# Kernel optimization log

Hardware: AMD Instinct MI355X
Metric: run time of the kernel (lower is better)

The kernel has to match this reference:

```python
import jax, jax.numpy as jnp
import numpy as np

E, M, B, S = 1024, 256, 4, 2048
LN_EPS = 1e-5

def _l2norm(x):
    # F.normalize(p=2, dim=-1, eps=1e-12)
    n = jnp.linalg.norm(x, axis=-1, keepdims=True)
    return x / jnp.maximum(n, 1e-12)

def _layernorm(x, g, b):
    mu = jnp.mean(x, axis=-1, keepdims=True)
    var = jnp.var(x, axis=-1, keepdims=True)
    return (x - mu) * jax.lax.rsqrt(var + LN_EPS) * g + b

def setup_inputs() -> dict:
    key = jax.random.key(0)
    ks = jax.random.split(key, 16)
    s = 0.02
    inp = {
        'x': jax.random.normal(ks[0], (B, S, E), jnp.float32),
        'memory': jnp.zeros((B, M, M), jnp.float32),
        'w_k': jax.random.normal(ks[1], (M, E), jnp.float32) * s,
        'b_k': jnp.zeros((M,), jnp.float32),
        'w_q': jax.random.normal(ks[2], (M, E), jnp.float32) * s,
        'b_q': jnp.zeros((M,), jnp.float32),
        'w_v': jax.random.normal(ks[3], (M, E), jnp.float32) * s,
        'b_v': jnp.zeros((M,), jnp.float32),
        'w_out': jax.random.normal(ks[4], (E, M), jnp.float32) * s,
        'b_out': jnp.zeros((E,), jnp.float32),
        'w_gw': jax.random.normal(ks[5], (1, E), jnp.float32) * s,
        'b_gw': jnp.full((1,), -2.0, jnp.float32),
        'w_gf': jax.random.normal(ks[6], (1, E), jnp.float32) * s,
        'b_gf': jnp.full((1,), 2.0, jnp.float32),
        'ln1_g': jnp.ones((E,), jnp.float32),
        'ln1_b': jnp.zeros((E,), jnp.float32),
        'ln2_g': jnp.ones((E,), jnp.float32),
        'ln2_b': jnp.zeros((E,), jnp.float32),
        'w_f1': jax.random.normal(ks[7], (4 * E, E), jnp.float32) * s,
        'b_f1': jnp.zeros((4 * E,), jnp.float32),
        'w_f2': jax.random.normal(ks[8], (E, 4 * E), jnp.float32) * s,
        'b_f2': jnp.zeros((E,), jnp.float32),
    }
    return inp

def reference(x, memory, w_k, b_k, w_q, b_q, w_v, b_v, w_out, b_out,
              w_gw, b_gw, w_gf, b_gf, ln1_g, ln1_b, ln2_g, ln2_b,
              w_f1, b_f1, w_f2, b_f2):
    xn = _layernorm(x, ln1_g, ln1_b)                      # [B,S,E]
    k_all = _l2norm(xn @ w_k.T + b_k)                     # [B,S,M]
    q_all = _l2norm(xn @ w_q.T + b_q)                     # [B,S,M]
    v_all = jnp.tanh(xn @ w_v.T + b_v)                    # [B,S,M]
    beta_all = jax.nn.sigmoid(xn @ w_gw.T + b_gw)         # [B,S,1]
    decay_all = jax.nn.sigmoid(xn @ w_gf.T + b_gf)        # [B,S,1]

    def step(mem, inps):
        k, q, v, beta, decay = inps                       # k,q,v:[B,M]; beta,decay:[B,1]
        readout = jnp.einsum('bij,bj->bi', mem, q)        # read BEFORE update
        assoc = v[:, :, None] * k[:, None, :]             # [B,M,M] outer product
        mem = decay[:, :, None] * mem + beta[:, :, None] * assoc
        return mem, readout

    seq = (jnp.swapaxes(k_all, 0, 1), jnp.swapaxes(q_all, 0, 1),
           jnp.swapaxes(v_all, 0, 1), jnp.swapaxes(beta_all, 0, 1),
           jnp.swapaxes(decay_all, 0, 1))
    new_memory, readouts = jax.lax.scan(step, memory, seq)  # readouts: [S,B,M]
    stacked = jnp.swapaxes(readouts, 0, 1)                  # [B,S,M]
    mixer_out = stacked @ w_out.T + b_out                   # [B,S,E]

    x = x + mixer_out
    h = _layernorm(x, ln2_g, ln2_b)
    ffn = jax.nn.gelu(h @ w_f1.T + b_f1, approximate=False) @ w_f2.T + b_f2
    x = x + ffn
    return (x, new_memory)
```

## Files before the change

kernel.cpp:

```cpp
#include <hip/hip_runtime.h>
#include <stdint.h>

#define E_DIM 1024
#define M_DIM 256
#define B_DIM 4
#define S_DIM 2048
#define NTOK  8192
#define CHUNK 64
#define NCHUNK 32
#define NCB   128

typedef unsigned short u16;
typedef unsigned int   u32;
typedef __attribute__((ext_vector_type(8))) short short8;
typedef __attribute__((ext_vector_type(4))) float floatx4;

#define OFF_WKQV   ((size_t)0)
#define OFF_WOUT   ((size_t)1572864)
#define OFF_WF1    ((size_t)2097152)
#define OFF_WF2    ((size_t)10485760)
#define OFF_BKQV   ((size_t)18874368)
#define OFF_BETA   ((size_t)18877440)
#define OFF_DECAY  ((size_t)18910208)
#define OFF_P      ((size_t)18942976)
#define OFF_WW     ((size_t)18976256)
#define OFF_ABUF   ((size_t)19009024)
#define OFF_XN     ((size_t)21106176)
#define OFF_KQV    ((size_t)37883392)
#define OFF_T      ((size_t)63049216)
#define OFF_STATES ((size_t)96603648)
#define OFF_RO     ((size_t)130158080)
#define OFF_H      OFF_XN
#define OFF_Y1     OFF_T
#define OFF_G      OFF_STATES

__device__ __forceinline__ u16 f2bf(float f) {
    union { float f; u32 u; } a; a.f = f;
    u32 u = a.u;
    return (u16)((u + 0x7fffu + ((u >> 16) & 1u)) >> 16);
}
__device__ __forceinline__ u32 pack2bf(float a, float b) {
    return (u32)f2bf(a) | ((u32)f2bf(b) << 16);
}
__device__ __forceinline__ float sigmoidf_(float x) { return 1.0f / (1.0f + expf(-x)); }

__device__ __forceinline__ void gload_lds16(const u16* g, u16* l) {
    __builtin_amdgcn_global_load_lds((const __attribute__((address_space(1))) void*)g,
                                     (__attribute__((address_space(3))) void*)l, 16, 0, 0);
}

__device__ __forceinline__ void block_reduce_2(float& a, float& b, float* red, int t) {
#pragma unroll
    for (int o = 32; o > 0; o >>= 1) { a += __shfl_xor(a, o); b += __shfl_xor(b, o); }
    if ((t & 63) == 0) { red[t >> 6] = a; red[4 + (t >> 6)] = b; }
    __syncthreads();
    a = red[0] + red[1] + red[2] + red[3];
    b = red[4] + red[5] + red[6] + red[7];
    __syncthreads();
}

__global__ void f2bf4_kernel(const float4* __restrict__ in, uint2* __restrict__ out, int n4) {
    int i = blockIdx.x * 256 + threadIdx.x;
    if (i < n4) {
        float4 v = in[i];
        uint2 o; o.x = pack2bf(v.x, v.y); o.y = pack2bf(v.z, v.w);
        out[i] = o;
    }
}
__global__ void pack_kqv_w(const float4* __restrict__ wk, const float4* __restrict__ wq,
                           const float4* __restrict__ wv, uint2* __restrict__ out) {
    int i = blockIdx.x * 256 + threadIdx.x;
    int sec = i >> 16;
    int off = i & 65535;
    const float4* src = (sec == 0) ? wk : ((sec == 1) ? wq : wv);
    float4 v = src[off];
    uint2 o; o.x = pack2bf(v.x, v.y); o.y = pack2bf(v.z, v.w);
    out[i] = o;
}
__global__ void pack_bias(const float* __restrict__ bk, const float* __restrict__ bq,
                          const float* __restrict__ bv, float* __restrict__ out) {
    int i = blockIdx.x * 256 + threadIdx.x;
    if (i < 256) out[i] = bk[i];
    else if (i < 512) out[i] = bq[i - 256];
    else out[i] = bv[i - 512];
}

__global__ __launch_bounds__(256) void ln1_gates(
    const float* __restrict__ x, const float* __restrict__ g, const float* __restrict__ b,
    const float* __restrict__ wgw, const float* __restrict__ bgw,
    const float* __restrict__ wgf, const float* __restrict__ bgf,
    u16* __restrict__ xn, float* __restrict__ beta, float* __restrict__ decay)
{
    __shared__ float red[8];
    const int row = blockIdx.x;
    const int t = threadIdx.x;
    const float4 v = ((const float4*)(x + (size_t)row * E_DIM))[t];
    float s  = v.x + v.y + v.z + v.w;
    float ss = v.x * v.x + v.y * v.y + v.z * v.z + v.w * v.w;
    block_reduce_2(s, ss, red, t);
    const float mean = s * (1.0f / E_DIM);
    const float var  = ss * (1.0f / E_DIM) - mean * mean;
    const float rstd = rsqrtf(var + 1e-5f);
    const float4 gg = ((const float4*)g)[t];
    const float4 bb = ((const float4*)b)[t];
    float4 xnv;
    xnv.x = (v.x - mean) * rstd * gg.x + bb.x;
    xnv.y = (v.y - mean) * rstd * gg.y + bb.y;
    xnv.z = (v.z - mean) * rstd * gg.z + bb.z;
    xnv.w = (v.w - mean) * rstd * gg.w + bb.w;
    uint2 o; o.x = pack2bf(xnv.x, xnv.y); o.y = pack2bf(xnv.z, xnv.w);
    ((uint2*)(xn + (size_t)row * E_DIM))[t] = o;
    const float4 w1 = ((const float4*)wgw)[t];
    const float4 w2 = ((const float4*)wgf)[t];
    float dg = xnv.x * w1.x + xnv.y * w1.y + xnv.z * w1.z + xnv.w * w1.w;
    float df = xnv.x * w2.x + xnv.y * w2.y + xnv.z * w2.z + xnv.w * w2.w;
    block_reduce_2(dg, df, red, t);
    if (t == 0) {
        beta[row]  = sigmoidf_(dg + bgw[0]);
        decay[row] = sigmoidf_(df + bgf[0]);
    }
}

__global__ __launch_bounds__(256) void ln2_kernel(
    const float* __restrict__ y1, const float* __restrict__ g, const float* __restrict__ b,
    u16* __restrict__ h)
{
    __shared__ float red[8];
    const int row = blockIdx.x;
    const int t = threadIdx.x;
    const float4 v = ((const float4*)(y1 + (size_t)row * E_DIM))[t];
    float s  = v.x + v.y + v.z + v.w;
    float ss = v.x * v.x + v.y * v.y + v.z * v.z + v.w * v.w;
    block_reduce_2(s, ss, red, t);
    const float mean = s * (1.0f / E_DIM);
    const float var  = ss * (1.0f / E_DIM) - mean * mean;
    const float rstd = rsqrtf(var + 1e-5f);
    const float4 gg = ((const float4*)g)[t];
    const float4 bb = ((const float4*)b)[t];
    float4 xnv;
    xnv.x = (v.x - mean) * rstd * gg.x + bb.x;
    xnv.y = (v.y - mean) * rstd * gg.y + bb.y;
    xnv.z = (v.z - mean) * rstd * gg.z + bb.z;
    xnv.w = (v.w - mean) * rstd * gg.w + bb.w;
    uint2 o; o.x = pack2bf(xnv.x, xnv.y); o.y = pack2bf(xnv.z, xnv.w);
    ((uint2*)(h + (size_t)row * E_DIM))[t] = o;
}

__global__ __launch_bounds__(256) void kqv_act(float* __restrict__ kqv) {
    __shared__ float red[8];
    const int row = blockIdx.x;
    const int t = threadIdx.x;
    float* p = kqv + (size_t)row * 768;
    float kv = p[t], qv = p[256 + t], vv = p[512 + t];
    float sk = kv * kv, sq = qv * qv;
    block_reduce_2(sk, sq, red, t);
    float nk = fmaxf(sqrtf(sk), 1e-12f);
    float nq = fmaxf(sqrtf(sq), 1e-12f);
    p[t]       = kv / nk;
    p[256 + t] = qv / nq;
    p[512 + t] = tanhf(vv);
}

__global__ void chunk_prep(const float* __restrict__ beta, const float* __restrict__ decay,
                           float* __restrict__ P, float* __restrict__ ww) {
    int cb = blockIdx.x;
    int b = cb >> 5, c = cb & 31;
    int tb = b * S_DIM + c * CHUNK;
    int j = threadIdx.x;
    __shared__ float d[64], bt[64], Ps[65];
    d[j]  = decay[tb + j];
    bt[j] = beta[tb + j];
    __syncthreads();
    if (j == 0) {
        float p = 1.0f; Ps[0] = 1.0f;
        for (int i = 0; i < 64; i++) { p *= d[i]; Ps[i + 1] = p; }
    }
    __syncthreads();
    P[cb * 65 + j] = Ps[j];
    if (j == 0) P[cb * 65 + 64] = Ps[64];
    ww[cb * 64 + j] = bt[j] / Ps[j + 1];
}

__global__ __launch_bounds__(256) void t_kernel(const float* __restrict__ kqv,
                                                const float* __restrict__ P,
                                                const float* __restrict__ ww,
                                                float* __restrict__ T) {
    int cb = blockIdx.y;
    int tile = blockIdx.x;
    int r0 = (tile >> 2) * 64, c0 = (tile & 3) * 64;
    int b = cb >> 5, c = cb & 31;
    int tb = b * S_DIM + c * CHUNK;
    float p64 = P[cb * 65 + 64];
    __shared__ float Vs[64][65], Ks[64][65];
    int t = threadIdx.x;
#pragma unroll
    for (int i = 0; i < 16; i++) {
        int idx = t + i * 256; int j = idx >> 6, col = idx & 63;
        float sc = ww[cb * 64 + j] * p64;
        Vs[j][col] = kqv[(size_t)(tb + j) * 768 + 512 + r0 + col] * sc;
        Ks[j][col] = kqv[(size_t)(tb + j) * 768 + 0   + c0 + col];
    }
    __syncthreads();
    int tr = t >> 4, tc = t & 15;
    float a[4][4] = {};
    for (int j = 0; j < 64; j++) {
        float vv[4], kk[4];
#pragma unroll
        for (int r = 0; r < 4; r++)  vv[r] = Vs[j][tr * 4 + r];
#pragma unroll
        for (int cc = 0; cc < 4; cc++) kk[cc] = Ks[j][tc * 4 + cc];
#pragma unroll
        for (int r = 0; r < 4; r++)
#pragma unroll
            for (int cc = 0; cc < 4; cc++) a[r][cc] += vv[r] * kk[cc];
    }
#pragma unroll
    for (int r = 0; r < 4; r++)
#pragma unroll
        for (int cc = 0; cc < 4; cc++)
            T[(size_t)cb * 65536 + (size_t)(r0 + tr * 4 + r) * 256 + (c0 + tc * 4 + cc)] = a[r][cc];
}

__global__ void mem_scan(const float* __restrict__ mem0, const float* __restrict__ T,
                         const float* __restrict__ P, float* __restrict__ states,
                         float* __restrict__ memOut) {
    int gid = blockIdx.x * 256 + threadIdx.x;
    int b = gid >> 16; int e = gid & 65535;
    float s = mem0[gid];
    for (int c = 0; c < NCHUNK; c++) {
        int cb = b * NCHUNK + c;
        states[(size_t)cb * 65536 + e] = s;
        s = P[cb * 65 + 64] * s + T[(size_t)cb * 65536 + e];
    }
    memOut[gid] = s;
}

__global__ __launch_bounds__(256) void qk_attn(const float* __restrict__ kqv,
                                               const float* __restrict__ P,
                                               const float* __restrict__ ww,
                                               float* __restrict__ Abuf) {
    int cb = blockIdx.x;
    int b = cb >> 5, c = cb & 31;
    int tb = b * S_DIM + c * CHUNK;
    __shared__ float Qs[64][65], Ks[64][65];
    int t = threadIdx.x;
    int tr = t >> 4, tc = t & 15;
    float acc[4][4] = {};
    for (int kt = 0; kt < 4; kt++) {
        __syncthreads();
#pragma unroll
        for (int i = 0; i < 16; i++) {
            int idx = t + i * 256; int rr = idx >> 6, cc2 = idx & 63;
            Qs[rr][cc2] = kqv[(size_t)(tb + rr) * 768 + 256 + kt * 64 + cc2];
            Ks[rr][cc2] = kqv[(size_t)(tb + rr) * 768 + 0   + kt * 64 + cc2];
        }
        __syncthreads();
        for (int kk = 0; kk < 64; kk++) {
            float qq[4], kx[4];
#pragma unroll
            for (int r = 0; r < 4; r++)  qq[r] = Qs[tr * 4 + r][kk];
#pragma unroll
            for (int cc = 0; cc < 4; cc++) kx[cc] = Ks[tc * 4 + cc][kk];
#pragma unroll
            for (int r = 0; r < 4; r++)
#pragma unroll
                for (int cc = 0; cc < 4; cc++) acc[r][cc] += qq[r] * kx[cc];
        }
    }
#pragma unroll
    for (int r = 0; r < 4; r++) {
#pragma unroll
        for (int cc = 0; cc < 4; cc++) {
            int i = tr * 4 + r, j = tc * 4 + cc;
            float v = (j < i) ? acc[r][cc] * (P[cb * 65 + i] * ww[cb * 64 + j]) : 0.0f;
            Abuf[(size_t)cb * 4096 + i * 64 + j] = v;
        }
    }
}

__global__ __launch_bounds__(256) void readout_k(const float* __restrict__ kqv,
                                                 const float* __restrict__ Abuf,
                                                 const float* __restrict__ states,
                                                 const float* __restrict__ P,
                                                 u16* __restrict__ ro) {
    int cb = blockIdx.y;
    int rt = blockIdx.x;
    int b = cb >> 5, c = cb & 31;
    int tb = b * S_DIM + c * CHUNK;
    int r0 = rt * 64;
    __shared__ float As[64][65], Vs[64][65], Qs[64][65], Ms[64][65];
    int t = threadIdx.x;
    int tr = t >> 4, tc = t & 15;
#pragma unroll
    for (int i = 0; i < 16; i++) {
        int idx = t + i * 256; int rr = idx >> 6, cc2 = idx & 63;
        As[rr][cc2] = Abuf[(size_t)cb * 4096 + rr * 64 + cc2];
        Vs[rr][cc2] = kqv[(size_t)(tb + rr) * 768 + 512 + r0 + cc2];
    }
    __syncthreads();
    float acc[4][4] = {};
    for (int j = 0; j < 64; j++) {
        float aa[4], vv[4];
#pragma unroll
        for (int r = 0; r < 4; r++)  aa[r] = As[tr * 4 + r][j];
#pragma unroll
        for (int cc = 0; cc < 4; cc++) vv[cc] = Vs[j][tc * 4 + cc];
#pragma unroll
        for (int r = 0; r < 4; r++)
#pragma unroll
            for (int cc = 0; cc < 4; cc++) acc[r][cc] += aa[r] * vv[cc];
    }
    float acc2[4][4] = {};
    for (int kt = 0; kt < 4; kt++) {
        __syncthreads();
#pragma unroll
        for (int i = 0; i < 16; i++) {
            int idx = t + i * 256; int rr = idx >> 6, cc2 = idx & 63;
            Qs[rr][cc2] = kqv[(size_t)(tb + rr) * 768 + 256 + kt * 64 + cc2];
            Ms[rr][cc2] = states[(size_t)cb * 65536 + (size_t)(r0 + rr) * 256 + kt * 64 + cc2];
        }
        __syncthreads();
        for (int kk = 0; kk < 64; kk++) {
            float qq[4], mm[4];
#pragma unroll
            for (int r = 0; r < 4; r++)  qq[r] = Qs[tr * 4 + r][kk];
#pragma unroll
            for (int cc = 0; cc < 4; cc++) mm[cc] = Ms[tc * 4 + cc][kk];
#pragma unroll
            for (int r = 0; r < 4; r++)
#pragma unroll
                for (int cc = 0; cc < 4; cc++) acc2[r][cc] += qq[r] * mm[cc];
        }
    }
#pragma unroll
    for (int r = 0; r < 4; r++) {
#pragma unroll
        for (int cc = 0; cc < 4; cc++) {
            int i = tr * 4 + r;
            float val = acc[r][cc] + P[cb * 65 + i] * acc2[r][cc];
            ro[(size_t)(tb + i) * 256 + r0 + tc * 4 + cc] = f2bf(val);
        }
    }
}

#define EPI_BIAS  0
#define EPI_RESID 1
#define EPI_GELU  2

template<int EPI>
__global__ __launch_bounds__(256) void gemm_bt(
    const u16* __restrict__ A, int lda,
    const u16* __restrict__ B, int ldb,
    const float* __restrict__ bias,
    const float* __restrict__ resid,
    float* __restrict__ outF, u16* __restrict__ outB,
    int ldc, int K)
{
    __shared__ u16 As[128 * 32];
    __shared__ u16 Bs[128 * 32];
    const int t = threadIdx.x;
    const int lane = t & 63;
    const int w = t >> 6;
    const int waveM = (w >> 1) * 64;
    const int waveN = (w & 1) * 64;
    const int m0 = blockIdx.y * 128;
    const int n0 = blockIdx.x * 128;

    const int r0i = t >> 2, c0i = (t & 3) * 8;
    const int r1i = (t + 256) >> 2, c1i = ((t + 256) & 3) * 8;
    const u16* Ag0 = A + (size_t)(m0 + r0i) * lda + c0i;
    const u16* Ag1 = A + (size_t)(m0 + r1i) * lda + c1i;
    const u16* Bg0 = B + (size_t)(n0 + r0i) * ldb + c0i;
    const u16* Bg1 = B + (size_t)(n0 + r1i) * ldb + c1i;
    u16* Al0 = As + t * 8;
    u16* Al1 = As + (t + 256) * 8;
    u16* Bl0 = Bs + t * 8;
    u16* Bl1 = Bs + (t + 256) * 8;

    floatx4 acc[4][4] = {};

    const int kg = (lane >> 4) * 8;
    const int rsel = lane & 15;

    for (int kt = 0; kt < K; kt += 32) {
        if (kt) __syncthreads();
        gload_lds16(Ag0 + kt, Al0);
        gload_lds16(Ag1 + kt, Al1);
        gload_lds16(Bg0 + kt, Bl0);
        gload_lds16(Bg1 + kt, Bl1);
        __syncthreads();
        short8 af[4], bfr[4];
#pragma unroll
        for (int i = 0; i < 4; i++)
            af[i] = *(const short8*)(As + (waveM + i * 16 + rsel) * 32 + kg);
#pragma unroll
        for (int j = 0; j < 4; j++)
            bfr[j] = *(const short8*)(Bs + (waveN + j * 16 + rsel) * 32 + kg);
#pragma unroll
        for (int i = 0; i < 4; i++)
#pragma unroll
            for (int j = 0; j < 4; j++)
                acc[i][j] = __builtin_amdgcn_mfma_f32_16x16x32_bf16(af[i], bfr[j], acc[i][j], 0, 0, 0);
    }

    const int rbase = (lane >> 4) * 4;
#pragma unroll
    for (int i = 0; i < 4; i++) {
#pragma unroll
        for (int j = 0; j < 4; j++) {
            const int col = n0 + waveN + j * 16 + rsel;
            const float bv = bias[col];
#pragma unroll
            for (int r = 0; r < 4; r++) {
                const int row = m0 + waveM + i * 16 + rbase + r;
                const size_t oidx = (size_t)row * ldc + col;
                float v = acc[i][j][r] + bv;
                if (EPI == EPI_BIAS) {
                    outF[oidx] = v;
                } else if (EPI == EPI_RESID) {
                    outF[oidx] = v + resid[oidx];
                } else {
                    float gl = 0.5f * v * (1.0f + erff(v * 0.70710678118654752f));
                    outB[oidx] = f2bf(gl);
                }
            }
        }
    }
}

extern "C" void kernel_launch(void* const* d_in, const int* in_sizes, int n_in,
                              void* d_out, int out_size, void* d_ws, size_t ws_size,
                              hipStream_t stream) {
    const float* x     = (const float*)d_in[0];
    const float* mem0  = (const float*)d_in[1];
    const float* w_k   = (const float*)d_in[2];
    const float* b_k   = (const float*)d_in[3];
    const float* w_q   = (const float*)d_in[4];
    const float* b_q   = (const float*)d_in[5];
    const float* w_v   = (const float*)d_in[6];
    const float* b_v   = (const float*)d_in[7];
    const float* w_out = (const float*)d_in[8];
    const float* b_out = (const float*)d_in[9];
    const float* w_gw  = (const float*)d_in[10];
    const float* b_gw  = (const float*)d_in[11];
    const float* w_gf  = (const float*)d_in[12];
    const float* b_gf  = (const float*)d_in[13];
    const float* ln1g  = (const float*)d_in[14];
    const float* ln1b  = (const float*)d_in[15];
    const float* ln2g  = (const float*)d_in[16];
    const float* ln2b  = (const float*)d_in[17];
    const float* w_f1  = (const float*)d_in[18];
    const float* b_f1  = (const float*)d_in[19];
    const float* w_f2  = (const float*)d_in[20];
    const float* b_f2  = (const float*)d_in[21];

    char* ws = (char*)d_ws;
    u16*   wkqv  = (u16*)(ws + OFF_WKQV);
    u16*   wout  = (u16*)(ws + OFF_WOUT);
    u16*   wf1   = (u16*)(ws + OFF_WF1);
    u16*   wf2   = (u16*)(ws + OFF_WF2);
    float* bkqv  = (float*)(ws + OFF_BKQV);
    float* beta  = (float*)(ws + OFF_BETA);
    float* decay = (float*)(ws + OFF_DECAY);
    float* P     = (float*)(ws + OFF_P);
    float* ww    = (float*)(ws + OFF_WW);
    float* Abuf  = (float*)(ws + OFF_ABUF);
    u16*   xn    = (u16*)(ws + OFF_XN);
    float* kqv   = (float*)(ws + OFF_KQV);
    float* T     = (float*)(ws + OFF_T);
    float* states= (float*)(ws + OFF_STATES);
    u16*   ro    = (u16*)(ws + OFF_RO);
    u16*   h     = (u16*)(ws + OFF_H);
    float* y1    = (float*)(ws + OFF_Y1);
    u16*   g     = (u16*)(ws + OFF_G);

    float* out_x   = (float*)d_out;
    float* out_mem = out_x + (size_t)NTOK * E_DIM;

    pack_kqv_w<<<768, 256, 0, stream>>>((const float4*)w_k, (const float4*)w_q,
                                        (const float4*)w_v, (uint2*)wkqv);
    f2bf4_kernel<<<256, 256, 0, stream>>>((const float4*)w_out, (uint2*)wout, 1024 * 256 / 4);
    f2bf4_kernel<<<4096, 256, 0, stream>>>((const float4*)w_f1, (uint2*)wf1, 4096 * 1024 / 4);
    f2bf4_kernel<<<4096, 256, 0, stream>>>((const float4*)w_f2, (uint2*)wf2, 1024 * 4096 / 4);
    pack_bias<<<3, 256, 0, stream>>>(b_k, b_q, b_v, bkqv);

    ln1_gates<<<NTOK, 256, 0, stream>>>(x, ln1g, ln1b, w_gw, b_gw, w_gf, b_gf, xn, beta, decay);

    gemm_bt<EPI_BIAS><<<dim3(6, 64), 256, 0, stream>>>(xn, 1024, wkqv, 1024, bkqv, nullptr,
                                                       kqv, nullptr, 768, 1024);
    kqv_act<<<NTOK, 256, 0, stream>>>(kqv);

    chunk_prep<<<NCB, 64, 0, stream>>>(beta, decay, P, ww);
    t_kernel<<<dim3(16, NCB), 256, 0, stream>>>(kqv, P, ww, T);
    mem_scan<<<1024, 256, 0, stream>>>(mem0, T, P, states, out_mem);
    qk_attn<<<NCB, 256, 0, stream>>>(kqv, P, ww, Abuf);
    readout_k<<<dim3(4, NCB), 256, 0, stream>>>(kqv, Abuf, states, P, ro);

    gemm_bt<EPI_RESID><<<dim3(8, 64), 256, 0, stream>>>(ro, 256, wout, 256, b_out, x,
                                                        y1, nullptr, 1024, 256);
    ln2_kernel<<<NTOK, 256, 0, stream>>>(y1, ln2g, ln2b, h);
    gemm_bt<EPI_GELU><<<dim3(32, 64), 256, 0, stream>>>(h, 1024, wf1, 1024, b_f1, nullptr,
                                                        nullptr, g, 4096, 1024);
    gemm_bt<EPI_RESID><<<dim3(8, 64), 256, 0, stream>>>(g, 4096, wf2, 4096, b_f2, y1,
                                                        out_x, nullptr, 1024, 4096);
}
```

Baseline: 537.1 us.

## Double-buffer LDS in gemm_bt and shrink M tile to 64 rows

```diff
diff --git a/kernel.cpp b/kernel.cpp
--- a/kernel.cpp
+++ b/kernel.cpp
@@ -356,48 +356,49 @@
     float* __restrict__ outF, u16* __restrict__ outB,
     int ldc, int K)
 {
-    __shared__ u16 As[128 * 32];
-    __shared__ u16 Bs[128 * 32];
+    __shared__ u16 As[2][64 * 32];
+    __shared__ u16 Bs[2][128 * 32];
     const int t = threadIdx.x;
     const int lane = t & 63;
     const int w = t >> 6;
-    const int waveM = (w >> 1) * 64;
+    const int waveM = (w >> 1) * 32;
     const int waveN = (w & 1) * 64;
-    const int m0 = blockIdx.y * 128;
+    const int m0 = blockIdx.y * 64;
     const int n0 = blockIdx.x * 128;
 
-    const int r0i = t >> 2, c0i = (t & 3) * 8;
-    const int r1i = (t + 256) >> 2, c1i = ((t + 256) & 3) * 8;
-    const u16* Ag0 = A + (size_t)(m0 + r0i) * lda + c0i;
-    const u16* Ag1 = A + (size_t)(m0 + r1i) * lda + c1i;
-    const u16* Bg0 = B + (size_t)(n0 + r0i) * ldb + c0i;
-    const u16* Bg1 = B + (size_t)(n0 + r1i) * ldb + c1i;
-    u16* Al0 = As + t * 8;
-    u16* Al1 = As + (t + 256) * 8;
-    u16* Bl0 = Bs + t * 8;
-    u16* Bl1 = Bs + (t + 256) * 8;
-
-    floatx4 acc[4][4] = {};
+    const int sr = t >> 2, sc = (t & 3) * 8;
+    const u16* Ag  = A + (size_t)(m0 + sr) * lda + sc;
+    const u16* Bg0 = B + (size_t)(n0 + sr) * ldb + sc;
+    const u16* Bg1 = B + (size_t)(n0 + 64 + sr) * ldb + sc;
+
+    floatx4 acc[2][4] = {};
 
     const int kg = (lane >> 4) * 8;
     const int rsel = lane & 15;
-
-    for (int kt = 0; kt < K; kt += 32) {
-        if (kt) __syncthreads();
-        gload_lds16(Ag0 + kt, Al0);
-        gload_lds16(Ag1 + kt, Al1);
-        gload_lds16(Bg0 + kt, Bl0);
-        gload_lds16(Bg1 + kt, Bl1);
+    const int NK = K >> 5;
+
+    gload_lds16(Ag, As[0] + t * 8);
+    gload_lds16(Bg0, Bs[0] + t * 8);
+    gload_lds16(Bg1, Bs[0] + (t + 256) * 8);
+
+    for (int kt = 0; kt < NK; kt++) {
         __syncthreads();
-        short8 af[4], bfr[4];
-#pragma unroll
-        for (int i = 0; i < 4; i++)
-            af[i] = *(const short8*)(As + (waveM + i * 16 + rsel) * 32 + kg);
+        const int cur = kt & 1;
+        if (kt + 1 < NK) {
+            const int kof = (kt + 1) * 32;
+            gload_lds16(Ag + kof, As[cur ^ 1] + t * 8);
+            gload_lds16(Bg0 + kof, Bs[cur ^ 1] + t * 8);
+            gload_lds16(Bg1 + kof, Bs[cur ^ 1] + (t + 256) * 8);
+        }
+        short8 af[2], bfr[4];
+#pragma unroll
+        for (int i = 0; i < 2; i++)
+            af[i] = *(const short8*)(As[cur] + (waveM + i * 16 + rsel) * 32 + kg);
 #pragma unroll
         for (int j = 0; j < 4; j++)
-            bfr[j] = *(const short8*)(Bs + (waveN + j * 16 + rsel) * 32 + kg);
-#pragma unroll
-        for (int i = 0; i < 4; i++)
+            bfr[j] = *(const short8*)(Bs[cur] + (waveN + j * 16 + rsel) * 32 + kg);
+#pragma unroll
+        for (int i = 0; i < 2; i++)
 #pragma unroll
             for (int j = 0; j < 4; j++)
                 acc[i][j] = __builtin_amdgcn_mfma_f32_16x16x32_bf16(af[i], bfr[j], acc[i][j], 0, 0, 0);
@@ -405,7 +406,7 @@
 
     const int rbase = (lane >> 4) * 4;
 #pragma unroll
-    for (int i = 0; i < 4; i++) {
+    for (int i = 0; i < 2; i++) {
 #pragma unroll
         for (int j = 0; j < 4; j++) {
             const int col = n0 + waveN + j * 16 + rsel;
@@ -486,8 +487,8 @@
 
     ln1_gates<<<NTOK, 256, 0, stream>>>(x, ln1g, ln1b, w_gw, b_gw, w_gf, b_gf, xn, beta, decay);
 
-    gemm_bt<EPI_BIAS><<<dim3(6, 64), 256, 0, stream>>>(xn, 1024, wkqv, 1024, bkqv, nullptr,
-                                                       kqv, nullptr, 768, 1024);
+    gemm_bt<EPI_BIAS><<<dim3(6, 128), 256, 0, stream>>>(xn, 1024, wkqv, 1024, bkqv, nullptr,
+                                                        kqv, nullptr, 768, 1024);
     kqv_act<<<NTOK, 256, 0, stream>>>(kqv);
 
     chunk_prep<<<NCB, 64, 0, stream>>>(beta, decay, P, ww);
@@ -496,11 +497,11 @@
     qk_attn<<<NCB, 256, 0, stream>>>(kqv, P, ww, Abuf);
     readout_k<<<dim3(4, NCB), 256, 0, stream>>>(kqv, Abuf, states, P, ro);
 
-    gemm_bt<EPI_RESID><<<dim3(8, 64), 256, 0, stream>>>(ro, 256, wout, 256, b_out, x,
-                                                        y1, nullptr, 1024, 256);
+    gemm_bt<EPI_RESID><<<dim3(8, 128), 256, 0, stream>>>(ro, 256, wout, 256, b_out, x,
+                                                         y1, nullptr, 1024, 256);
     ln2_kernel<<<NTOK, 256, 0, stream>>>(y1, ln2g, ln2b, h);
-    gemm_bt<EPI_GELU><<<dim3(32, 64), 256, 0, stream>>>(h, 1024, wf1, 1024, b_f1, nullptr,
-                                                        nullptr, g, 4096, 1024);
-    gemm_bt<EPI_RESID><<<dim3(8, 64), 256, 0, stream>>>(g, 4096, wf2, 4096, b_f2, y1,
-                                                        out_x, nullptr, 1024, 4096);
-}
+    gemm_bt<EPI_GELU><<<dim3(32, 128), 256, 0, stream>>>(h, 1024, wf1, 1024, b_f1, nullptr,
+                                                         nullptr, g, 4096, 1024);
+    gemm_bt<EPI_RESID><<<dim3(8, 128), 256, 0, stream>>>(g, 4096, wf2, 4096, b_f2, y1,
+                                                         out_x, nullptr, 1024, 4096);
+}
```

Result: no change. 539.3 us (+0.4%).
